# Kernel optimization log

Measured on AMD Instinct MI355X. Metric: run time of the kernel, lower is better.

## Reference

```python
import jax, jax.numpy as jnp
import numpy as np

C = 96          # channels (= output_dim)
NUM_HEADS = 6
DILS = (1, 2, 3)
KS_ATT = 3      # dilate-attention kernel size
KS_COR = 5      # self-correlation kernel size
PAD_COR = 2
LN_EPS = 1e-5


def _unfold(x, k, dil, pad):
    # torch.nn.Unfold(kernel=k, dilation=dil, padding=pad, stride=1)
    # x: [B, C, H, W] -> [B, C, k*k, H, W] (channel-major, kernel row-major)
    B, c, H, W = x.shape
    xp = jnp.pad(x, ((0, 0), (0, 0), (pad, pad), (pad, pad)))
    patches = [xp[:, :, i * dil:i * dil + H, j * dil:j * dil + W]
               for i in range(k) for j in range(k)]
    return jnp.stack(patches, axis=2)


def _layernorm(x, g, b):
    m = jnp.mean(x, axis=-1, keepdims=True)
    v = jnp.mean((x - m) ** 2, axis=-1, keepdims=True)
    return (x - m) * jax.lax.rsqrt(v + LN_EPS) * g + b


def _dilate_attn(q, k, v, dil, head_dim, scale):
    # q,k,v: [B, cb, H, W] with cb = C // num_dilation
    B, cb, H, W = q.shape
    heads = cb // head_dim
    qf = q.reshape(B, heads, head_dim, H * W)                                  # bhdn
    kp = _unfold(k, KS_ATT, dil, dil).reshape(B, heads, head_dim, KS_ATT * KS_ATT, H * W)
    attn = jax.nn.softmax(jnp.einsum('bhdn,bhdkn->bhnk', qf, kp) * scale, axis=-1)
    vp = _unfold(v, KS_ATT, dil, dil).reshape(B, heads, head_dim, KS_ATT * KS_ATT, H * W)
    out = jnp.einsum('bhnk,bhdkn->bnhd', attn, vp)                             # [B,HW,heads,hd]
    return out.reshape(B, H, W, cb)


def _forward(x, g1, b1, Wqkv, bqkv, Wproj, bproj, g2, b2, W1, bm1, W2, bm2):
    B, Cc, H, W = x.shape
    nd = len(DILS)
    head_dim = Cc // NUM_HEADS
    scale = head_dim ** (-0.5)

    xh = jnp.transpose(x, (0, 2, 3, 1))                                        # [B,H,W,C]

    # --- MultiDilatelocalAttention block ---
    y = _layernorm(xh, g1, b1)
    qkv = jnp.einsum('bhwc,oc->bhwo', y, Wqkv) + bqkv                          # 1x1 conv == linear
    qkv = jnp.transpose(qkv, (0, 3, 1, 2)).reshape(B, 3, nd, Cc // nd, H, W)
    outs = []
    for i, d in enumerate(DILS):
        outs.append(_dilate_attn(qkv[:, 0, i], qkv[:, 1, i], qkv[:, 2, i], d, head_dim, scale))
    a = jnp.concatenate(outs, axis=-1)                                         # dilation-major channels
    a = a @ Wproj.T + bproj
    xh = xh + a

    # --- MLP block ---
    z = _layernorm(xh, g2, b2)
    z = jax.nn.gelu(z @ W1.T + bm1, approximate=False) @ W2.T + bm2
    xh = xh + z

    # --- self-correlation ---
    xc = jnp.transpose(xh, (0, 3, 1, 2))                                       # [B,C,H,W]
    xc = jax.nn.relu(xc)
    nrm = jnp.sqrt(jnp.sum(xc * xc, axis=1, keepdims=True))
    xc = xc / jnp.maximum(nrm, 1e-12)                                          # F.normalize dim=1
    pat = _unfold(xc, KS_COR, 1, PAD_COR)                                      # [B,C,25,H,W]
    out = pat.reshape(B, Cc, KS_COR, KS_COR, H, W) * xc[:, :, None, None]
    return jnp.transpose(out, (0, 1, 4, 5, 2, 3))                              # [B,C,H,W,5,5]


def setup_inputs() -> dict:
    key = jax.random.key(0)
    ks = jax.random.split(key, 8)
    B, H, W = 8, 64, 64
    s = 0.02
    return {
        'x': jax.random.normal(ks[0], (B, C, H, W), jnp.float32),
        'g1': jnp.ones((C,), jnp.float32),
        'b1': jnp.zeros((C,), jnp.float32),
        'Wqkv': jax.random.normal(ks[1], (3 * C, C), jnp.float32) * s,
        'bqkv': jnp.zeros((3 * C,), jnp.float32),
        'Wproj': jax.random.normal(ks[2], (C, C), jnp.float32) * s,
        'bproj': jnp.zeros((C,), jnp.float32),
        'g2': jnp.ones((C,), jnp.float32),
        'b2': jnp.zeros((C,), jnp.float32),
        'W1': jax.random.normal(ks[3], (4 * C, C), jnp.float32) * s,
        'bm1': jnp.zeros((4 * C,), jnp.float32),
        'W2': jax.random.normal(ks[4], (C, 4 * C), jnp.float32) * s,
        'bm2': jnp.zeros((C,), jnp.float32),
    }


def reference(x, g1, b1, Wqkv, bqkv, Wproj, bproj, g2, b2, W1, bm1, W2, bm2):
    return _forward(x, g1, b1, Wqkv, bqkv, Wproj, bproj, g2, b2, W1, bm1, W2, bm2)
```

## Files before the change

kernel.cpp:

```cpp
#include <hip/hip_runtime.h>
#include <math.h>

#define NN 4096
#define BN 32768
#define CSTR 66

using short8 = __attribute__((ext_vector_type(8))) short;
using f32x4  = __attribute__((ext_vector_type(4))) float;
typedef unsigned short ushort_t;

__device__ inline unsigned f2bfu(float f) {
    unsigned u = __builtin_bit_cast(unsigned, f);
    u += 0x7FFFu + ((u >> 16) & 1u);
    return u >> 16;
}
__device__ inline ushort_t f2bf(float f) { return (ushort_t)f2bfu(f); }
__device__ inline unsigned pack2(float a, float b) { return f2bfu(a) | (f2bfu(b) << 16); }
__device__ inline float bflo(unsigned u) { return __builtin_bit_cast(float, u << 16); }
__device__ inline float bfhi(unsigned u) { return __builtin_bit_cast(float, u & 0xFFFF0000u); }

__device__ inline float gelu_f(float v) {
    float xx = v * 0.70710678118654752f;
    float a  = fabsf(xx);
    float t  = 1.0f / (1.0f + 0.3275911f * a);
    float p  = t*(0.254829592f + t*(-0.284496736f + t*(1.421413741f + t*(-1.453152027f + t*1.061405429f))));
    float erfv = 1.0f - p * __expf(-xx*xx);
    erfv = copysignf(erfv, xx);
    return 0.5f * v * (1.0f + erfv);
}

__device__ inline void stage_w(const unsigned* __restrict__ wbf, int stage,
                               ushort_t* dst, int wv, int lane) {
    const unsigned* src = wbf + (long)stage * 5120 + lane * 4;
    #pragma unroll
    for (int i = 0; i < 5; ++i) {
        int chunk = wv + 4 * i;
        __builtin_amdgcn_global_load_lds(
            (const __attribute__((address_space(1))) unsigned*)(src + chunk * 256),
            (__attribute__((address_space(3))) unsigned*)(dst + chunk * 512),
            16, 0, 0);
    }
}

__global__ __launch_bounds__(256) void k0_pack(
    const float* __restrict__ Wqkv, const float* __restrict__ Wproj,
    const float* __restrict__ W1, const float* __restrict__ W2,
    unsigned* __restrict__ wbf)
{
    int d = blockIdx.x * 256 + threadIdx.x;
    int s = d / 5120, r = d - s * 5120;
    int o = r / 52, qp = r - o * 52;
    unsigned val = 0u;
    if (o < 96 && qp < 48) {
        int q = qp * 2;
        float2 w2;
        if (s == 0)      w2 = *(const float2*)&Wqkv[(long)o * 96 + q];
        else if (s == 1) w2 = *(const float2*)&Wqkv[(long)(96 + o) * 96 + q];
        else if (s == 2) w2 = *(const float2*)&Wqkv[(long)(192 + o) * 96 + q];
        else if (s == 3) w2 = *(const float2*)&Wproj[(long)o * 96 + q];
        else if (((s - 4) & 1) == 0) { int kb = (s - 4) >> 1; w2 = *(const float2*)&W1[(long)(kb * 96 + o) * 96 + q]; }
        else                         { int kb = (s - 4) >> 1; w2 = *(const float2*)&W2[(long)o * 384 + kb * 96 + q]; }
        val = pack2(w2.x, w2.y);
    }
    wbf[d] = val;
}

__global__ __launch_bounds__(256, 2) void k1_ln_kv(
    const float* __restrict__ x, const float* __restrict__ g1, const float* __restrict__ b1,
    const float* __restrict__ bqkv, const unsigned* __restrict__ wbf,
    unsigned* __restrict__ kvt32)
{
    __shared__ __align__(16) float    Cs[96 * CSTR];
    __shared__ __align__(16) ushort_t As[64 * 104];
    __shared__ __align__(16) ushort_t Bs[2][10240];
    __shared__ float lnm[64], lnr[64];
    const int tid = threadIdx.x;
    const int bid = blockIdx.x;
    const int wg  = ((bid & 7) << 6) | (bid >> 3);
    const long bn0 = (long)wg << 6;
    const int b  = (int)(bn0 >> 12);
    const int n0 = (int)(bn0 & 4095);
    const int lane = tid & 63, wv = tid >> 6;
    const int ln = lane & 15, qd = lane >> 4;

    stage_w(wbf, 1, &Bs[0][0], wv, lane);
    stage_w(wbf, 2, &Bs[1][0], wv, lane);
    for (int i = 0; i < 24; ++i) {
        int idx = i * 256 + tid;
        int c = idx >> 6, p = idx & 63;
        Cs[c * CSTR + p] = x[((long)(b * 96 + c) << 12) + n0 + p];
    }
    __syncthreads();
    {
        int p = tid >> 2, part = tid & 3, c0 = part * 24;
        float s = 0.f, ss = 0.f;
        for (int c = c0; c < c0 + 24; ++c) { float v = Cs[c*CSTR + p]; s += v; ss += v*v; }
        s  += __shfl_xor(s, 1);  s  += __shfl_xor(s, 2);
        ss += __shfl_xor(ss, 1); ss += __shfl_xor(ss, 2);
        float m = s * (1.f/96.f);
        float rstd = rsqrtf(ss * (1.f/96.f) - m*m + 1e-5f);
        if (part == 0) { lnm[p] = m; lnr[p] = rstd; }
    }
    __syncthreads();
    for (int i = 0; i < 12; ++i) {
        int idx = i * 256 + tid;
        int p = idx / 48, cp = idx % 48;
        float m = lnm[p], rs = lnr[p];
        int c = 2 * cp;
        *(unsigned*)&As[p * 104 + 2*cp] =
            pack2((Cs[c*CSTR + p]     - m) * rs * g1[c]   + b1[c],
                  (Cs[(c+1)*CSTR + p] - m) * rs * g1[c+1] + b1[c+1]);
    }
    __syncthreads();
    f32x4 acck[6], accv[6];
    #pragma unroll
    for (int t = 0; t < 6; ++t) { acck[t] = (f32x4){0.f,0.f,0.f,0.f}; accv[t] = (f32x4){0.f,0.f,0.f,0.f}; }
    #pragma unroll
    for (int kc = 0; kc < 3; ++kc) {
        short8 a = *(const short8*)&As[(wv*16 + ln)*104 + kc*32 + qd*8];
        #pragma unroll
        for (int t = 0; t < 6; ++t) {
            short8 bf = *(const short8*)&Bs[0][(t*16 + ln)*104 + kc*32 + qd*8];
            acck[t] = __builtin_amdgcn_mfma_f32_16x16x32_bf16(a, bf, acck[t], 0, 0, 0);
        }
    }
    #pragma unroll
    for (int t = 0; t < 6; ++t)
        #pragma unroll
        for (int r = 0; r < 4; ++r)
            Cs[(t*16 + ln)*CSTR + (wv*16 + qd*4 + r)] = acck[t][r];
    __syncthreads();
    #pragma unroll
    for (int kc = 0; kc < 3; ++kc) {
        short8 a = *(const short8*)&As[(wv*16 + ln)*104 + kc*32 + qd*8];
        #pragma unroll
        for (int t = 0; t < 6; ++t) {
            short8 bf = *(const short8*)&Bs[1][(t*16 + ln)*104 + kc*32 + qd*8];
            accv[t] = __builtin_amdgcn_mfma_f32_16x16x32_bf16(a, bf, accv[t], 0, 0, 0);
        }
    }
    for (int i = 0; i < 12; ++i) {
        int idx = i * 256 + tid;
        int cp = idx / 64, p = idx % 64;
        int c = 2 * cp;
        kvt32[((long)(b*96 + cp) << 12) + n0 + p] =
            pack2(Cs[c*CSTR + p] + bqkv[96 + c], Cs[(c+1)*CSTR + p] + bqkv[96 + c + 1]);
    }
    __syncthreads();
    #pragma unroll
    for (int t = 0; t < 6; ++t)
        #pragma unroll
        for (int r = 0; r < 4; ++r)
            Cs[(t*16 + ln)*CSTR + (wv*16 + qd*4 + r)] = accv[t][r];
    __syncthreads();
    for (int i = 0; i < 12; ++i) {
        int idx = i * 256 + tid;
        int cp = idx / 64, p = idx % 64;
        int c = 2 * cp;
        kvt32[((long)(b*96 + 48 + cp) << 12) + n0 + p] =
            pack2(Cs[c*CSTR + p] + bqkv[192 + c], Cs[(c+1)*CSTR + p] + bqkv[192 + c + 1]);
    }
}

__global__ __launch_bounds__(256, 2) void k2345(
    const unsigned* __restrict__ kvt32, const float* __restrict__ x,
    const float* __restrict__ g1, const float* __restrict__ b1,
    const float* __restrict__ bqkv, const unsigned* __restrict__ wbf,
    const float* __restrict__ bproj,
    const float* __restrict__ g2, const float* __restrict__ b2,
    const float* __restrict__ bm1, const float* __restrict__ bm2,
    float* __restrict__ xcn)
{
    __shared__ __align__(16) float    Cs[96 * CSTR];
    __shared__ __align__(16) ushort_t As[64 * 104];
    __shared__ __align__(16) ushort_t Bs[2][10240];
    __shared__ float lnm[64], lnr[64];
    ushort_t* Hs = (ushort_t*)Cs;
    const int tid = threadIdx.x;
    const int bid = blockIdx.x;
    const int wg  = ((bid & 7) << 6) | (bid >> 3);
    const long bn0 = (long)wg << 6;
    const int b  = (int)(bn0 >> 12);
    const int n0 = (int)(bn0 & 4095);
    const int h0 = n0 >> 6;
    const int lane = tid & 63, wv = tid >> 6;
    const int ln = lane & 15, qd = lane >> 4;

    stage_w(wbf, 0, &Bs[0][0], wv, lane);
    stage_w(wbf, 3, &Bs[1][0], wv, lane);
    for (int i = 0; i < 24; ++i) {
        int idx = i * 256 + tid;
        int c = idx >> 6, p = idx & 63;
        Cs[c * CSTR + p] = x[((long)(b * 96 + c) << 12) + n0 + p];
    }
    __syncthreads();
    {
        int p = tid >> 2, part = tid & 3, c0 = part * 24;
        float s = 0.f, ss = 0.f;
        for (int c = c0; c < c0 + 24; ++c) { float v = Cs[c*CSTR + p]; s += v; ss += v*v; }
        s  += __shfl_xor(s, 1);  s  += __shfl_xor(s, 2);
        ss += __shfl_xor(ss, 1); ss += __shfl_xor(ss, 2);
        float m = s * (1.f/96.f);
        float rstd = rsqrtf(ss * (1.f/96.f) - m*m + 1e-5f);
        if (part == 0) { lnm[p] = m; lnr[p] = rstd; }
    }
    __syncthreads();
    for (int i = 0; i < 12; ++i) {
        int idx = i * 256 + tid;
        int p = idx / 48, cp = idx % 48;
        float m = lnm[p], rs = lnr[p];
        int c = 2 * cp;
        *(unsigned*)&As[p * 104 + 2*cp] =
            pack2((Cs[c*CSTR + p]     - m) * rs * g1[c]   + b1[c],
                  (Cs[(c+1)*CSTR + p] - m) * rs * g1[c+1] + b1[c+1]);
    }
    __syncthreads();
    {
        f32x4 acc[6];
        #pragma unroll
        for (int t = 0; t < 6; ++t) acc[t] = (f32x4){0.f,0.f,0.f,0.f};
        #pragma unroll
        for (int kc = 0; kc < 3; ++kc) {
            short8 a = *(const short8*)&As[(wv*16 + ln)*104 + kc*32 + qd*8];
            #pragma unroll
            for (int t = 0; t < 6; ++t) {
                short8 bf = *(const short8*)&Bs[0][(t*16 + ln)*104 + kc*32 + qd*8];
                acc[t] = __builtin_amdgcn_mfma_f32_16x16x32_bf16(a, bf, acc[t], 0, 0, 0);
            }
        }
        #pragma unroll
        for (int t = 0; t < 6; ++t) {
            float bias = bqkv[t*16 + ln];
            #pragma unroll
            for (int r = 0; r < 4; ++r)
                As[(wv*16 + qd*4 + r)*104 + t*16 + ln] = f2bf(acc[t][r] + bias);
        }
    }
    __syncthreads();
    stage_w(wbf, 4, &Bs[0][0], wv, lane);
    for (int it = 0; it < 2; ++it) {
        int item = it * 256 + tid;
        if (item < 384) {
            int p = item & 63;
            int r = item >> 6;
            int head = r & 1, di = r >> 1;
            int dil = di + 1;
            int cp0 = di*16 + head*8;
            const unsigned* K = kvt32 + ((long)(b*96 +      cp0) << 12);
            const unsigned* V = kvt32 + ((long)(b*96 + 48 + cp0) << 12);
            int w = p;

            float q[16];
            #pragma unroll
            for (int j = 0; j < 8; ++j) {
                unsigned u = *(const unsigned*)&As[p * 104 + 2*(cp0 + j)];
                q[2*j] = bflo(u); q[2*j+1] = bfhi(u);
            }
            float logits[9];
            #pragma unroll
            for (int ki = 0; ki < 3; ++ki)
                #pragma unroll
                for (int kj = 0; kj < 3; ++kj) {
                    int hh = h0 + (ki-1)*dil, ww = w + (kj-1)*dil;
                    float l = 0.f;
                    if ((unsigned)hh < 64u && (unsigned)ww < 64u) {
                        int nn = (hh << 6) + ww;
                        #pragma unroll
                        for (int j = 0; j < 8; ++j) {
                            unsigned u = K[((long)j << 12) + nn];
                            l += q[2*j] * bflo(u) + q[2*j+1] * bfhi(u);
                        }
                    }
                    logits[ki*3 + kj] = l * 0.25f;
                }
            float m = logits[0];
            #pragma unroll
            for (int k = 1; k < 9; ++k) m = fmaxf(m, logits[k]);
            float e[9], s = 0.f;
            #pragma unroll
            for (int k = 0; k < 9; ++k) { e[k] = __expf(logits[k] - m); s += e[k]; }
            float inv = 1.f / s;
            float o[16];
            #pragma unroll
            for (int d = 0; d < 16; ++d) o[d] = 0.f;
            #pragma unroll
            for (int ki = 0; ki < 3; ++ki)
                #pragma unroll
                for (int kj = 0; kj < 3; ++kj) {
                    int hh = h0 + (ki-1)*dil, ww = w + (kj-1)*dil;
                    if ((unsigned)hh < 64u && (unsigned)ww < 64u) {
                        int nn = (hh << 6) + ww;
                        float wgt = e[ki*3 + kj] * inv;
                        #pragma unroll
                        for (int j = 0; j < 8; ++j) {
                            unsigned u = V[((long)j << 12) + nn];
                            o[2*j]   += wgt * bflo(u);
                            o[2*j+1] += wgt * bfhi(u);
                        }
                    }
                }
            #pragma unroll
            for (int j = 0; j < 8; ++j)
                *(unsigned*)&As[p * 104 + 2*(cp0 + j)] = pack2(o[2*j], o[2*j+1]);
        }
    }
    __syncthreads();
    float resid[24];
    {
        f32x4 acc[6];
        #pragma unroll
        for (int t = 0; t < 6; ++t) acc[t] = (f32x4){0.f,0.f,0.f,0.f};
        #pragma unroll
        for (int kc = 0; kc < 3; ++kc) {
            short8 a = *(const short8*)&As[(wv*16 + ln)*104 + kc*32 + qd*8];
            #pragma unroll
            for (int t = 0; t < 6; ++t) {
                short8 bf = *(const short8*)&Bs[1][(t*16 + ln)*104 + kc*32 + qd*8];
                acc[t] = __builtin_amdgcn_mfma_f32_16x16x32_bf16(a, bf, acc[t], 0, 0, 0);
            }
        }
        #pragma unroll
        for (int t = 0; t < 6; ++t) {
            int oc = t*16 + ln;
            float bias = bproj[oc];
            #pragma unroll
            for (int r = 0; r < 4; ++r) {
                int p = wv*16 + qd*4 + r;
                float v = acc[t][r] + bias + Cs[oc*CSTR + p];
                resid[t*4 + r] = v;
                Cs[oc*CSTR + p] = v;
            }
        }
    }
    __syncthreads();
    stage_w(wbf, 5, &Bs[1][0], wv, lane);
    {
        int p = tid >> 2, part = tid & 3, c0 = part * 24;
        float s = 0.f, ss = 0.f;
        for (int c = c0; c < c0 + 24; ++c) { float v = Cs[c*CSTR + p]; s += v; ss += v*v; }
        s  += __shfl_xor(s, 1);  s  += __shfl_xor(s, 2);
        ss += __shfl_xor(ss, 1); ss += __shfl_xor(ss, 2);
        float m = s * (1.f/96.f);
        float rstd = rsqrtf(ss * (1.f/96.f) - m*m + 1e-5f);
        if (part == 0) { lnm[p] = m; lnr[p] = rstd; }
    }
    __syncthreads();
    for (int i = 0; i < 12; ++i) {
        int idx = i * 256 + tid;
        int p = idx / 48, cp = idx % 48;
        float m = lnm[p], rs = lnr[p];
        int c = 2 * cp;
        *(unsigned*)&As[p * 104 + 2*cp] =
            pack2((Cs[c*CSTR + p]     - m) * rs * g2[c]   + b2[c],
                  (Cs[(c+1)*CSTR + p] - m) * rs * g2[c+1] + b2[c+1]);
    }
    __syncthreads();
    f32x4 acc2[6];
    #pragma unroll
    for (int t = 0; t < 6; ++t) acc2[t] = (f32x4){0.f,0.f,0.f,0.f};
    for (int kb = 0; kb < 4; ++kb) {
        f32x4 acch[6];
        #pragma unroll
        for (int t = 0; t < 6; ++t) acch[t] = (f32x4){0.f,0.f,0.f,0.f};
        #pragma unroll
        for (int kc = 0; kc < 3; ++kc) {
            short8 a = *(const short8*)&As[(wv*16 + ln)*104 + kc*32 + qd*8];
            #pragma unroll
            for (int t = 0; t < 6; ++t) {
                short8 bf = *(const short8*)&Bs[0][(t*16 + ln)*104 + kc*32 + qd*8];
                acch[t] = __builtin_amdgcn_mfma_f32_16x16x32_bf16(a, bf, acch[t], 0, 0, 0);
            }
        }
        #pragma unroll
        for (int t = 0; t < 6; ++t) {
            float bias = bm1[kb*96 + t*16 + ln];
            #pragma unroll
            for (int r = 0; r < 4; ++r)
                Hs[(wv*16 + qd*4 + r)*104 + t*16 + ln] = f2bf(gelu_f(acch[t][r] + bias));
        }
        __syncthreads();
        if (kb < 3) stage_w(wbf, 6 + 2*kb, &Bs[0][0], wv, lane);
        #pragma unroll
        for (int kc = 0; kc < 3; ++kc) {
            short8 a = *(const short8*)&Hs[(wv*16 + ln)*104 + kc*32 + qd*8];
            #pragma unroll
            for (int t = 0; t < 6; ++t) {
                short8 bf = *(const short8*)&Bs[1][(t*16 + ln)*104 + kc*32 + qd*8];
                acc2[t] = __builtin_amdgcn_mfma_f32_16x16x32_bf16(a, bf, acc2[t], 0, 0, 0);
            }
        }
        __syncthreads();
        if (kb < 3) stage_w(wbf, 7 + 2*kb, &Bs[1][0], wv, lane);
    }
    #pragma unroll
    for (int t = 0; t < 6; ++t) {
        int oc = t*16 + ln;
        float bias = bm2[oc];
        #pragma unroll
        for (int r = 0; r < 4; ++r) {
            int p = wv*16 + qd*4 + r;
            float v = acc2[t][r] + bias + resid[t*4 + r];
            Cs[oc*CSTR + p] = fmaxf(v, 0.f);
        }
    }
    __syncthreads();
    {
        int p = tid >> 2, part = tid & 3, c0 = part * 24;
        float ss = 0.f;
        for (int c = c0; c < c0 + 24; ++c) { float v = Cs[c*CSTR + p]; ss += v*v; }
        ss += __shfl_xor(ss, 1); ss += __shfl_xor(ss, 2);
        if (part == 0) lnr[p] = 1.f / fmaxf(sqrtf(ss), 1e-12f);
    }
    __syncthreads();
    for (int i = 0; i < 12; ++i) {
        int idx = i * 256 + tid;
        int p = idx / 48, cp = idx % 48;
        float inv = lnr[p];
        float2 v = make_float2(Cs[(2*cp)*CSTR + p] * inv, Cs[(2*cp+1)*CSTR + p] * inv);
        *(float2*)&xcn[(bn0 + p) * 96 + 2*cp] = v;
    }
}

__global__ __launch_bounds__(256) void k6_selfcorr(
    const float* __restrict__ xcn, float* __restrict__ out)
{
    __shared__ float xt[5 * 20 * 97];
    const int tid = threadIdx.x;
    const int wc = blockIdx.x;
    const int h  = blockIdx.y;
    const int b  = blockIdx.z;
    const int w0 = wc * 16;

    for (int i = 0; i < 38; ++i) {
        int idx = i * 256 + tid;
        if (idx < 9600) {
            int r = idx / (20 * 96);
            int rem = idx - r * (20 * 96);
            int wi = rem / 96, c = rem - wi * 96;
            int hh = h + r - 2, ww = w0 + wi - 2;
            float v = 0.f;
            if ((unsigned)hh < 64u && (unsigned)ww < 64u)
                v = xcn[(((long)b << 12) + (hh << 6) + ww) * 96 + c];
            xt[(r * 20 + wi) * 97 + c] = v;
        }
    }
    __syncthreads();
    f32x4* out4 = (f32x4*)out;
    const long ob4 = (long)b * 2457600 + (long)h * 400 + wc * 100;
    for (int i = 0; i < 38; ++i) {
        int idx = i * 256 + tid;
        if (idx < 9600) {
            int c = idx / 100;
            int r4 = idx - c * 100;
            f32x4 v;
            #pragma unroll
            for (int j = 0; j < 4; ++j) {
                int r = r4 * 4 + j;
                int lw = r / 25, k = r - lw * 25;
                int ki = k / 5, kj = k - ki * 5;
                float center = xt[(42 + lw) * 97 + c];
                float neigh  = xt[(ki * 20 + lw + kj) * 97 + c];
                v[j] = center * neigh;
            }
            __builtin_nontemporal_store(v, &out4[ob4 + (long)c * 25600 + r4]);
        }
    }
}

extern "C" void kernel_launch(void* const* d_in, const int* in_sizes, int n_in,
                              void* d_out, int out_size, void* d_ws, size_t ws_size,
                              hipStream_t stream)
{
    const float* x     = (const float*)d_in[0];
    const float* g1    = (const float*)d_in[1];
    const float* b1    = (const float*)d_in[2];
    const float* Wqkv  = (const float*)d_in[3];
    const float* bqkv  = (const float*)d_in[4];
    const float* Wproj = (const float*)d_in[5];
    const float* bproj = (const float*)d_in[6];
    const float* g2    = (const float*)d_in[7];
    const float* b2    = (const float*)d_in[8];
    const float* W1    = (const float*)d_in[9];
    const float* bm1   = (const float*)d_in[10];
    const float* W2    = (const float*)d_in[11];
    const float* bm2   = (const float*)d_in[12];
    float* out = (float*)d_out;

    char* w = (char*)d_ws;
    unsigned* wbf   = (unsigned*)w;  w += 12 * 20480;
    unsigned* kvt32 = (unsigned*)w;  w += (size_t)BN * 192 * 2;
    float*    xcn   = (float*)w;

    k0_pack    <<<240, 256, 0, stream>>>(Wqkv, Wproj, W1, W2, wbf);
    k1_ln_kv   <<<BN / 64, 256, 0, stream>>>(x, g1, b1, bqkv, wbf, kvt32);
    k2345      <<<BN / 64, 256, 0, stream>>>(kvt32, x, g1, b1, bqkv, wbf,
                                             bproj, g2, b2, bm1, bm2, xcn);
    k6_selfcorr<<<dim3(4, 64, 8), 256, 0, stream>>>(xcn, out);
}
```

Baseline: 406.2 us.

## Compute Q in first kernel, store K/V pixel-major for vectorized attention loads

The Q projection moves from the attention kernel into the LN/QKV kernel, which now writes a padded bf16 Q tile image that the second kernel copies straight into LDS. This removes the duplicate LayerNorm and Q GEMM from the second kernel. K/V are now stored pixel-major (96 packed words per pixel) instead of channel-major, so each neighbour's 16-dim head slice is read with two 16-byte loads instead of eight strided 4-byte loads. The x tile load is also vectorized to float4. The cost is an extra global round trip for Q and a less coalesced K/V store in the first kernel.

```diff
diff --git a/kernel.cpp b/kernel.cpp
--- a/kernel.cpp
+++ b/kernel.cpp
@@ -41,6 +41,44 @@
             16, 0, 0);
     }
 }
+
+__device__ inline float dotk16(const unsigned* kv, const float* q) {
+    const uint4 a = *(const uint4*)kv;
+    const uint4 b = *(const uint4*)(kv + 4);
+    float l;
+    l  = q[0]*bflo(a.x)  + q[1]*bfhi(a.x);
+    l += q[2]*bflo(a.y)  + q[3]*bfhi(a.y);
+    l += q[4]*bflo(a.z)  + q[5]*bfhi(a.z);
+    l += q[6]*bflo(a.w)  + q[7]*bfhi(a.w);
+    l += q[8]*bflo(b.x)  + q[9]*bfhi(b.x);
+    l += q[10]*bflo(b.y) + q[11]*bfhi(b.y);
+    l += q[12]*bflo(b.z) + q[13]*bfhi(b.z);
+    l += q[14]*bflo(b.w) + q[15]*bfhi(b.w);
+    return l;
+}
+__device__ inline void accv16(const unsigned* kv, float wgt, float* o) {
+    const uint4 a = *(const uint4*)kv;
+    const uint4 b = *(const uint4*)(kv + 4);
+    o[0]  += wgt*bflo(a.x);  o[1]  += wgt*bfhi(a.x);
+    o[2]  += wgt*bflo(a.y);  o[3]  += wgt*bfhi(a.y);
+    o[4]  += wgt*bflo(a.z);  o[5]  += wgt*bfhi(a.z);
+    o[6]  += wgt*bflo(a.w);  o[7]  += wgt*bfhi(a.w);
+    o[8]  += wgt*bflo(b.x);  o[9]  += wgt*bfhi(b.x);
+    o[10] += wgt*bflo(b.y);  o[11] += wgt*bfhi(b.y);
+    o[12] += wgt*bflo(b.z);  o[13] += wgt*bfhi(b.z);
+    o[14] += wgt*bflo(b.w);  o[15] += wgt*bfhi(b.w);
+}
+
+#define MFMA_GEMM6(ACC, APTR, BPTR)                                              \
+    _Pragma("unroll")                                                            \
+    for (int kc = 0; kc < 3; ++kc) {                                             \
+        short8 a_ = *(const short8*)&(APTR)[(wv*16 + ln)*104 + kc*32 + qd*8];    \
+        _Pragma("unroll")                                                        \
+        for (int t = 0; t < 6; ++t) {                                            \
+            short8 b_ = *(const short8*)&(BPTR)[(t*16 + ln)*104 + kc*32 + qd*8]; \
+            ACC[t] = __builtin_amdgcn_mfma_f32_16x16x32_bf16(a_, b_, ACC[t], 0, 0, 0); \
+        }                                                                        \
+    }
 
 __global__ __launch_bounds__(256) void k0_pack(
     const float* __restrict__ Wqkv, const float* __restrict__ Wproj,
@@ -65,10 +103,10 @@
     wbf[d] = val;
 }
 
-__global__ __launch_bounds__(256, 2) void k1_ln_kv(
+__global__ __launch_bounds__(256, 2) void k1_ln_qkv(
     const float* __restrict__ x, const float* __restrict__ g1, const float* __restrict__ b1,
     const float* __restrict__ bqkv, const unsigned* __restrict__ wbf,
-    unsigned* __restrict__ kvt32)
+    unsigned* __restrict__ kvt32, unsigned* __restrict__ qimg)
 {
     __shared__ __align__(16) float    Cs[96 * CSTR];
     __shared__ __align__(16) ushort_t As[64 * 104];
@@ -83,12 +121,14 @@
     const int lane = tid & 63, wv = tid >> 6;
     const int ln = lane & 15, qd = lane >> 4;
 
-    stage_w(wbf, 1, &Bs[0][0], wv, lane);
-    stage_w(wbf, 2, &Bs[1][0], wv, lane);
-    for (int i = 0; i < 24; ++i) {
-        int idx = i * 256 + tid;
-        int c = idx >> 6, p = idx & 63;
-        Cs[c * CSTR + p] = x[((long)(b * 96 + c) << 12) + n0 + p];
+    stage_w(wbf, 0, &Bs[0][0], wv, lane);
+    stage_w(wbf, 1, &Bs[1][0], wv, lane);
+    for (int i = 0; i < 6; ++i) {
+        int idx = i * 256 + tid;
+        int c = idx >> 4, p4 = idx & 15;
+        float4 v = *(const float4*)&x[((long)(b * 96 + c) << 12) + n0 + p4 * 4];
+        float* dst = &Cs[c * CSTR + p4 * 4];
+        dst[0] = v.x; dst[1] = v.y; dst[2] = v.z; dst[3] = v.w;
     }
     __syncthreads();
     {
@@ -112,60 +152,66 @@
                   (Cs[(c+1)*CSTR + p] - m) * rs * g1[c+1] + b1[c+1]);
     }
     __syncthreads();
-    f32x4 acck[6], accv[6];
-    #pragma unroll
-    for (int t = 0; t < 6; ++t) { acck[t] = (f32x4){0.f,0.f,0.f,0.f}; accv[t] = (f32x4){0.f,0.f,0.f,0.f}; }
-    #pragma unroll
-    for (int kc = 0; kc < 3; ++kc) {
-        short8 a = *(const short8*)&As[(wv*16 + ln)*104 + kc*32 + qd*8];
-        #pragma unroll
-        for (int t = 0; t < 6; ++t) {
-            short8 bf = *(const short8*)&Bs[0][(t*16 + ln)*104 + kc*32 + qd*8];
-            acck[t] = __builtin_amdgcn_mfma_f32_16x16x32_bf16(a, bf, acck[t], 0, 0, 0);
-        }
-    }
+    f32x4 acc[6];
+    #pragma unroll
+    for (int t = 0; t < 6; ++t) acc[t] = (f32x4){0.f,0.f,0.f,0.f};
+    MFMA_GEMM6(acc, As, Bs[0]);
     #pragma unroll
     for (int t = 0; t < 6; ++t)
         #pragma unroll
         for (int r = 0; r < 4; ++r)
-            Cs[(t*16 + ln)*CSTR + (wv*16 + qd*4 + r)] = acck[t][r];
-    __syncthreads();
-    #pragma unroll
-    for (int kc = 0; kc < 3; ++kc) {
-        short8 a = *(const short8*)&As[(wv*16 + ln)*104 + kc*32 + qd*8];
-        #pragma unroll
-        for (int t = 0; t < 6; ++t) {
-            short8 bf = *(const short8*)&Bs[1][(t*16 + ln)*104 + kc*32 + qd*8];
-            accv[t] = __builtin_amdgcn_mfma_f32_16x16x32_bf16(a, bf, accv[t], 0, 0, 0);
-        }
-    }
+            Cs[(t*16 + ln)*CSTR + (wv*16 + qd*4 + r)] = acc[t][r];
+    __syncthreads();
+    stage_w(wbf, 2, &Bs[0][0], wv, lane);
+    for (int i = 0; i < 13; ++i) {
+        int idx = i * 256 + tid;
+        int p = idx / 52, cp = idx - p * 52;
+        unsigned val = 0u;
+        if (cp < 48) {
+            int c = 2 * cp;
+            val = pack2(Cs[c*CSTR + p] + bqkv[c], Cs[(c+1)*CSTR + p] + bqkv[c+1]);
+        }
+        qimg[(long)wg * 3328 + idx] = val;
+    }
+    #pragma unroll
+    for (int t = 0; t < 6; ++t) acc[t] = (f32x4){0.f,0.f,0.f,0.f};
+    MFMA_GEMM6(acc, As, Bs[1]);
+    __syncthreads();
+    #pragma unroll
+    for (int t = 0; t < 6; ++t)
+        #pragma unroll
+        for (int r = 0; r < 4; ++r)
+            Cs[(t*16 + ln)*CSTR + (wv*16 + qd*4 + r)] = acc[t][r];
+    __syncthreads();
     for (int i = 0; i < 12; ++i) {
         int idx = i * 256 + tid;
-        int cp = idx / 64, p = idx % 64;
+        int p = idx / 48, cp = idx % 48;
         int c = 2 * cp;
-        kvt32[((long)(b*96 + cp) << 12) + n0 + p] =
+        kvt32[(bn0 + p) * 96 + cp] =
             pack2(Cs[c*CSTR + p] + bqkv[96 + c], Cs[(c+1)*CSTR + p] + bqkv[96 + c + 1]);
     }
+    #pragma unroll
+    for (int t = 0; t < 6; ++t) acc[t] = (f32x4){0.f,0.f,0.f,0.f};
+    MFMA_GEMM6(acc, As, Bs[0]);
     __syncthreads();
     #pragma unroll
     for (int t = 0; t < 6; ++t)
         #pragma unroll
         for (int r = 0; r < 4; ++r)
-            Cs[(t*16 + ln)*CSTR + (wv*16 + qd*4 + r)] = accv[t][r];
+            Cs[(t*16 + ln)*CSTR + (wv*16 + qd*4 + r)] = acc[t][r];
     __syncthreads();
     for (int i = 0; i < 12; ++i) {
         int idx = i * 256 + tid;
-        int cp = idx / 64, p = idx % 64;
+        int p = idx / 48, cp = idx % 48;
         int c = 2 * cp;
-        kvt32[((long)(b*96 + 48 + cp) << 12) + n0 + p] =
+        kvt32[(bn0 + p) * 96 + 48 + cp] =
             pack2(Cs[c*CSTR + p] + bqkv[192 + c], Cs[(c+1)*CSTR + p] + bqkv[192 + c + 1]);
     }
 }
 
 __global__ __launch_bounds__(256, 2) void k2345(
-    const unsigned* __restrict__ kvt32, const float* __restrict__ x,
-    const float* __restrict__ g1, const float* __restrict__ b1,
-    const float* __restrict__ bqkv, const unsigned* __restrict__ wbf,
+    const unsigned* __restrict__ kvt32, const unsigned* __restrict__ qimg,
+    const float* __restrict__ x, const unsigned* __restrict__ wbf,
     const float* __restrict__ bproj,
     const float* __restrict__ g2, const float* __restrict__ b2,
     const float* __restrict__ bm1, const float* __restrict__ bm2,
@@ -186,14 +232,105 @@
     const int lane = tid & 63, wv = tid >> 6;
     const int ln = lane & 15, qd = lane >> 4;
 
-    stage_w(wbf, 0, &Bs[0][0], wv, lane);
-    stage_w(wbf, 3, &Bs[1][0], wv, lane);
-    for (int i = 0; i < 24; ++i) {
-        int idx = i * 256 + tid;
-        int c = idx >> 6, p = idx & 63;
-        Cs[c * CSTR + p] = x[((long)(b * 96 + c) << 12) + n0 + p];
-    }
-    __syncthreads();
+    stage_w(wbf, 3, &Bs[0][0], wv, lane);
+    stage_w(wbf, 4, &Bs[1][0], wv, lane);
+    {
+        const unsigned* src = qimg + (long)wg * 3328 + lane * 4;
+        #pragma unroll
+        for (int i = 0; i < 4; ++i) {
+            int chunk = wv + 4 * i;
+            if (chunk < 13)
+                __builtin_amdgcn_global_load_lds(
+                    (const __attribute__((address_space(1))) unsigned*)(src + chunk * 256),
+                    (__attribute__((address_space(3))) unsigned*)((ushort_t*)As + chunk * 512),
+                    16, 0, 0);
+        }
+    }
+    for (int i = 0; i < 6; ++i) {
+        int idx = i * 256 + tid;
+        int c = idx >> 4, p4 = idx & 15;
+        float4 v = *(const float4*)&x[((long)(b * 96 + c) << 12) + n0 + p4 * 4];
+        float* dst = &Cs[c * CSTR + p4 * 4];
+        dst[0] = v.x; dst[1] = v.y; dst[2] = v.z; dst[3] = v.w;
+    }
+    __syncthreads();
+    const unsigned* KV = kvt32 + (long)b * 4096 * 96;
+    for (int it = 0; it < 2; ++it) {
+        int item = it * 256 + tid;
+        if (item < 384) {
+            int p = item & 63;
+            int r = item >> 6;
+            int head = r & 1, di = r >> 1;
+            int dil = di + 1;
+            int cp0 = di*16 + head*8;
+            int w = p;
+
+            float q[16];
+            #pragma unroll
+            for (int j = 0; j < 8; ++j) {
+                unsigned u = *(const unsigned*)&As[p * 104 + 2*(cp0 + j)];
+                q[2*j] = bflo(u); q[2*j+1] = bfhi(u);
+            }
+            float logits[9];
+            #pragma unroll
+            for (int ki = 0; ki < 3; ++ki)
+                #pragma unroll
+                for (int kj = 0; kj < 3; ++kj) {
+                    int hh = h0 + (ki-1)*dil, ww = w + (kj-1)*dil;
+                    float l = 0.f;
+                    if ((unsigned)hh < 64u && (unsigned)ww < 64u) {
+                        int nn = (hh << 6) + ww;
+                        l = dotk16(KV + (long)nn * 96 + cp0, q);
+                    }
+                    logits[ki*3 + kj] = l * 0.25f;
+                }
+            float m = logits[0];
+            #pragma unroll
+            for (int k = 1; k < 9; ++k) m = fmaxf(m, logits[k]);
+            float e[9], s = 0.f;
+            #pragma unroll
+            for (int k = 0; k < 9; ++k) { e[k] = __expf(logits[k] - m); s += e[k]; }
+            float inv = 1.f / s;
+            float o[16];
+            #pragma unroll
+            for (int d = 0; d < 16; ++d) o[d] = 0.f;
+            #pragma unroll
+            for (int ki = 0; ki < 3; ++ki)
+                #pragma unroll
+                for (int kj = 0; kj < 3; ++kj) {
+                    int hh = h0 + (ki-1)*dil, ww = w + (kj-1)*dil;
+                    if ((unsigned)hh < 64u && (unsigned)ww < 64u) {
+                        int nn = (hh << 6) + ww;
+                        accv16(KV + (long)nn * 96 + 48 + cp0, e[ki*3 + kj] * inv, o);
+                    }
+                }
+            #pragma unroll
+            for (int j = 0; j < 8; ++j)
+                *(unsigned*)&As[p * 104 + 2*(cp0 + j)] = pack2(o[2*j], o[2*j+1]);
+        }
+    }
+    __syncthreads();
+    float resid[24];
+    {
+        f32x4 acc[6];
+        #pragma unroll
+        for (int t = 0; t < 6; ++t) acc[t] = (f32x4){0.f,0.f,0.f,0.f};
+        MFMA_GEMM6(acc, As, Bs[0]);
+        #pragma unroll
+        for (int t = 0; t < 6; ++t) {
+            int oc = t*16 + ln;
+            float bias = bproj[oc];
+            #pragma unroll
+            for (int r = 0; r < 4; ++r) {
+                int p = wv*16 + qd*4 + r;
+                float v = acc[t][r] + bias + Cs[oc*CSTR + p];
+                resid[t*4 + r] = v;
+                Cs[oc*CSTR + p] = v;
+            }
+        }
+    }
+    __syncthreads();
+    stage_w(wbf, 5, &Bs[0][0], wv, lane);
     {
         int p = tid >> 2, part = tid & 3, c0 = part * 24;
         float s = 0.f, ss = 0.f;
@@ -211,146 +348,6 @@
         float m = lnm[p], rs = lnr[p];
         int c = 2 * cp;
         *(unsigned*)&As[p * 104 + 2*cp] =
-            pack2((Cs[c*CSTR + p]     - m) * rs * g1[c]   + b1[c],
-                  (Cs[(c+1)*CSTR + p] - m) * rs * g1[c+1] + b1[c+1]);
-    }
-    __syncthreads();
-    {
-        f32x4 acc[6];
-        #pragma unroll
-        for (int t = 0; t < 6; ++t) acc[t] = (f32x4){0.f,0.f,0.f,0.f};
-        #pragma unroll
-        for (int kc = 0; kc < 3; ++kc) {
-            short8 a = *(const short8*)&As[(wv*16 + ln)*104 + kc*32 + qd*8];
-            #pragma unroll
-            for (int t = 0; t < 6; ++t) {
-                short8 bf = *(const short8*)&Bs[0][(t*16 + ln)*104 + kc*32 + qd*8];
-                acc[t] = __builtin_amdgcn_mfma_f32_16x16x32_bf16(a, bf, acc[t], 0, 0, 0);
-            }
-        }
-        #pragma unroll
-        for (int t = 0; t < 6; ++t) {
-            float bias = bqkv[t*16 + ln];
-            #pragma unroll
-            for (int r = 0; r < 4; ++r)
-                As[(wv*16 + qd*4 + r)*104 + t*16 + ln] = f2bf(acc[t][r] + bias);
-        }
-    }
-    __syncthreads();
-    stage_w(wbf, 4, &Bs[0][0], wv, lane);
-    for (int it = 0; it < 2; ++it) {
-        int item = it * 256 + tid;
-        if (item < 384) {
-            int p = item & 63;
-            int r = item >> 6;
-            int head = r & 1, di = r >> 1;
-            int dil = di + 1;
-            int cp0 = di*16 + head*8;
-            const unsigned* K = kvt32 + ((long)(b*96 +      cp0) << 12);
-            const unsigned* V = kvt32 + ((long)(b*96 + 48 + cp0) << 12);
-            int w = p;
-
-            float q[16];
-            #pragma unroll
-            for (int j = 0; j < 8; ++j) {
-                unsigned u = *(const unsigned*)&As[p * 104 + 2*(cp0 + j)];
-                q[2*j] = bflo(u); q[2*j+1] = bfhi(u);
-            }
-            float logits[9];
-            #pragma unroll
-            for (int ki = 0; ki < 3; ++ki)
-                #pragma unroll
-                for (int kj = 0; kj < 3; ++kj) {
-                    int hh = h0 + (ki-1)*dil, ww = w + (kj-1)*dil;
-                    float l = 0.f;
-                    if ((unsigned)hh < 64u && (unsigned)ww < 64u) {
-                        int nn = (hh << 6) + ww;
-                        #pragma unroll
-                        for (int j = 0; j < 8; ++j) {
-                            unsigned u = K[((long)j << 12) + nn];
-                            l += q[2*j] * bflo(u) + q[2*j+1] * bfhi(u);
-                        }
-                    }
-                    logits[ki*3 + kj] = l * 0.25f;
-                }
-            float m = logits[0];
-            #pragma unroll
-            for (int k = 1; k < 9; ++k) m = fmaxf(m, logits[k]);
-            float e[9], s = 0.f;
-            #pragma unroll
-            for (int k = 0; k < 9; ++k) { e[k] = __expf(logits[k] - m); s += e[k]; }
-            float inv = 1.f / s;
-            float o[16];
-            #pragma unroll
-            for (int d = 0; d < 16; ++d) o[d] = 0.f;
-            #pragma unroll
-            for (int ki = 0; ki < 3; ++ki)
-                #pragma unroll
-                for (int kj = 0; kj < 3; ++kj) {
-                    int hh = h0 + (ki-1)*dil, ww = w + (kj-1)*dil;
-                    if ((unsigned)hh < 64u && (unsigned)ww < 64u) {
-                        int nn = (hh << 6) + ww;
-                        float wgt = e[ki*3 + kj] * inv;
-                        #pragma unroll
-                        for (int j = 0; j < 8; ++j) {
-                            unsigned u = V[((long)j << 12) + nn];
-                            o[2*j]   += wgt * bflo(u);
-                            o[2*j+1] += wgt * bfhi(u);
-                        }
-                    }
-                }
-            #pragma unroll
-            for (int j = 0; j < 8; ++j)
-                *(unsigned*)&As[p * 104 + 2*(cp0 + j)] = pack2(o[2*j], o[2*j+1]);
-        }
-    }
-    __syncthreads();
-    float resid[24];
-    {
-        f32x4 acc[6];
-        #pragma unroll
-        for (int t = 0; t < 6; ++t) acc[t] = (f32x4){0.f,0.f,0.f,0.f};
-        #pragma unroll
-        for (int kc = 0; kc < 3; ++kc) {
-            short8 a = *(const short8*)&As[(wv*16 + ln)*104 + kc*32 + qd*8];
-            #pragma unroll
-            for (int t = 0; t < 6; ++t) {
-                short8 bf = *(const short8*)&Bs[1][(t*16 + ln)*104 + kc*32 + qd*8];
-                acc[t] = __builtin_amdgcn_mfma_f32_16x16x32_bf16(a, bf, acc[t], 0, 0, 0);
-            }
-        }
-        #pragma unroll
-        for (int t = 0; t < 6; ++t) {
-            int oc = t*16 + ln;
-            float bias = bproj[oc];
-            #pragma unroll
-            for (int r = 0; r < 4; ++r) {
-                int p = wv*16 + qd*4 + r;
-                float v = acc[t][r] + bias + Cs[oc*CSTR + p];
-                resid[t*4 + r] = v;
-                Cs[oc*CSTR + p] = v;
-            }
-        }
-    }
-    __syncthreads();
-    stage_w(wbf, 5, &Bs[1][0], wv, lane);
-    {
-        int p = tid >> 2, part = tid & 3, c0 = part * 24;
-        float s = 0.f, ss = 0.f;
-        for (int c = c0; c < c0 + 24; ++c) { float v = Cs[c*CSTR + p]; s += v; ss += v*v; }
-        s  += __shfl_xor(s, 1);  s  += __shfl_xor(s, 2);
-        ss += __shfl_xor(ss, 1); ss += __shfl_xor(ss, 2);
-        float m = s * (1.f/96.f);
-        float rstd = rsqrtf(ss * (1.f/96.f) - m*m + 1e-5f);
-        if (part == 0) { lnm[p] = m; lnr[p] = rstd; }
-    }
-    __syncthreads();
-    for (int i = 0; i < 12; ++i) {
-        int idx = i * 256 + tid;
-        int p = idx / 48, cp = idx % 48;
-        float m = lnm[p], rs = lnr[p];
-        int c = 2 * cp;
-        *(unsigned*)&As[p * 104 + 2*cp] =
             pack2((Cs[c*CSTR + p]     - m) * rs * g2[c]   + b2[c],
                   (Cs[(c+1)*CSTR + p] - m) * rs * g2[c+1] + b2[c+1]);
     }
@@ -362,15 +359,7 @@
         f32x4 acch[6];
         #pragma unroll
         for (int t = 0; t < 6; ++t) acch[t] = (f32x4){0.f,0.f,0.f,0.f};
-        #pragma unroll
-        for (int kc = 0; kc < 3; ++kc) {
-            short8 a = *(const short8*)&As[(wv*16 + ln)*104 + kc*32 + qd*8];
-            #pragma unroll
-            for (int t = 0; t < 6; ++t) {
-                short8 bf = *(const short8*)&Bs[0][(t*16 + ln)*104 + kc*32 + qd*8];
-                acch[t] = __builtin_amdgcn_mfma_f32_16x16x32_bf16(a, bf, acch[t], 0, 0, 0);
-            }
-        }
+        MFMA_GEMM6(acch, As, Bs[1]);
         #pragma unroll
         for (int t = 0; t < 6; ++t) {
             float bias = bm1[kb*96 + t*16 + ln];
@@ -379,18 +368,10 @@
                 Hs[(wv*16 + qd*4 + r)*104 + t*16 + ln] = f2bf(gelu_f(acch[t][r] + bias));
         }
         __syncthreads();
-        if (kb < 3) stage_w(wbf, 6 + 2*kb, &Bs[0][0], wv, lane);
-        #pragma unroll
-        for (int kc = 0; kc < 3; ++kc) {
-            short8 a = *(const short8*)&Hs[(wv*16 + ln)*104 + kc*32 + qd*8];
-            #pragma unroll
-            for (int t = 0; t < 6; ++t) {
-                short8 bf = *(const short8*)&Bs[1][(t*16 + ln)*104 + kc*32 + qd*8];
-                acc2[t] = __builtin_amdgcn_mfma_f32_16x16x32_bf16(a, bf, acc2[t], 0, 0, 0);
-            }
-        }
+        if (kb < 3) stage_w(wbf, 6 + 2*kb, &Bs[1][0], wv, lane);
+        MFMA_GEMM6(acc2, Hs, Bs[0]);
         __syncthreads();
-        if (kb < 3) stage_w(wbf, 7 + 2*kb, &Bs[1][0], wv, lane);
+        if (kb < 3) stage_w(wbf, 7 + 2*kb, &Bs[0][0], wv, lane);
     }
     #pragma unroll
     for (int t = 0; t < 6; ++t) {
@@ -488,12 +469,13 @@
 
     char* w = (char*)d_ws;
     unsigned* wbf   = (unsigned*)w;  w += 12 * 20480;
-    unsigned* kvt32 = (unsigned*)w;  w += (size_t)BN * 192 * 2;
+    unsigned* kvt32 = (unsigned*)w;  w += (size_t)BN * 96 * 4;
+    unsigned* qimg  = (unsigned*)w;  w += (size_t)512 * 3328 * 4;
     float*    xcn   = (float*)w;
 
     k0_pack    <<<240, 256, 0, stream>>>(Wqkv, Wproj, W1, W2, wbf);
-    k1_ln_kv   <<<BN / 64, 256, 0, stream>>>(x, g1, b1, bqkv, wbf, kvt32);
-    k2345      <<<BN / 64, 256, 0, stream>>>(kvt32, x, g1, b1, bqkv, wbf,
+    k1_ln_qkv  <<<BN / 64, 256, 0, stream>>>(x, g1, b1, bqkv, wbf, kvt32, qimg);
+    k2345      <<<BN / 64, 256, 0, stream>>>(kvt32, qimg, x, wbf,
                                              bproj, g2, b2, bm1, bm2, xcn);
     k6_selfcorr<<<dim3(4, 64, 8), 256, 0, stream>>>(xcn, out);
 }
```

Result: no change. 409.6 us (+0.8%).

## Compute LayerNorm directly into MFMA register fragments and vectorize global loads

Applied to the files above, without the earlier changes.

Each LayerNorm now has every lane compute its row's statistics with cross-lane shuffles and build the bf16 A-operand fragments in registers. This removes the shared-memory As staging, the separate stats pass and several barriers in k1 and k2345. The x tile loads in k1/k2345 and the xcn halo load in k6 switch to float4 global reads. The cost is more register pressure (24 floats per lane plus fragments), which could hurt occupancy under the 2-blocks launch bound.

```diff
diff --git a/kernel.cpp b/kernel.cpp
--- a/kernel.cpp
+++ b/kernel.cpp
@@ -41,6 +41,56 @@
             16, 0, 0);
     }
 }
+
+#define MFMA_GEMM6(ACC, APTR, BPTR)                                              \
+    _Pragma("unroll")                                                            \
+    for (int kc = 0; kc < 3; ++kc) {                                             \
+        short8 a_ = *(const short8*)&(APTR)[(wv*16 + ln)*104 + kc*32 + qd*8];    \
+        _Pragma("unroll")                                                        \
+        for (int t = 0; t < 6; ++t) {                                            \
+            short8 b_ = *(const short8*)&(BPTR)[(t*16 + ln)*104 + kc*32 + qd*8]; \
+            ACC[t] = __builtin_amdgcn_mfma_f32_16x16x32_bf16(a_, b_, ACC[t], 0, 0, 0); \
+        }                                                                        \
+    }
+
+#define MFMA_GEMM6R(ACC, AF, BPTR)                                               \
+    _Pragma("unroll")                                                            \
+    for (int kc = 0; kc < 3; ++kc) {                                             \
+        _Pragma("unroll")                                                        \
+        for (int t = 0; t < 6; ++t) {                                            \
+            short8 b_ = *(const short8*)&(BPTR)[(t*16 + ln)*104 + kc*32 + qd*8]; \
+            ACC[t] = __builtin_amdgcn_mfma_f32_16x16x32_bf16(AF[kc], b_, ACC[t], 0, 0, 0); \
+        }                                                                        \
+    }
+
+#define LN_FRAGS(AF, CS, G, B)                                                   \
+    {                                                                            \
+        const int p_ = wv*16 + ln;                                               \
+        float xv_[24]; float s_ = 0.f, ss_ = 0.f;                                \
+        _Pragma("unroll")                                                        \
+        for (int kc = 0; kc < 3; ++kc)                                           \
+            _Pragma("unroll")                                                    \
+            for (int j = 0; j < 8; ++j) {                                        \
+                float v_ = (CS)[(kc*32 + qd*8 + j)*CSTR + p_];                   \
+                xv_[kc*8+j] = v_; s_ += v_; ss_ += v_*v_;                        \
+            }                                                                    \
+        s_  += __shfl_xor(s_, 16);  s_  += __shfl_xor(s_, 32);                   \
+        ss_ += __shfl_xor(ss_, 16); ss_ += __shfl_xor(ss_, 32);                  \
+        float m_ = s_ * (1.f/96.f);                                              \
+        float rs_ = rsqrtf(ss_ * (1.f/96.f) - m_*m_ + 1e-5f);                    \
+        _Pragma("unroll")                                                        \
+        for (int kc = 0; kc < 3; ++kc)                                           \
+            _Pragma("unroll")                                                    \
+            for (int h = 0; h < 2; ++h) {                                        \
+                int c0_ = kc*32 + qd*8 + h*4;                                    \
+                float4 g4_ = *(const float4*)&(G)[c0_];                          \
+                float4 b4_ = *(const float4*)&(B)[c0_];                          \
+                (AF)[kc][h*4+0] = (short)f2bf((xv_[kc*8+h*4+0]-m_)*rs_*g4_.x + b4_.x); \
+                (AF)[kc][h*4+1] = (short)f2bf((xv_[kc*8+h*4+1]-m_)*rs_*g4_.y + b4_.y); \
+                (AF)[kc][h*4+2] = (short)f2bf((xv_[kc*8+h*4+2]-m_)*rs_*g4_.z + b4_.z); \
+                (AF)[kc][h*4+3] = (short)f2bf((xv_[kc*8+h*4+3]-m_)*rs_*g4_.w + b4_.w); \
+            }                                                                    \
+    }
 
 __global__ __launch_bounds__(256) void k0_pack(
     const float* __restrict__ Wqkv, const float* __restrict__ Wproj,
@@ -71,9 +121,7 @@
     unsigned* __restrict__ kvt32)
 {
     __shared__ __align__(16) float    Cs[96 * CSTR];
-    __shared__ __align__(16) ushort_t As[64 * 104];
     __shared__ __align__(16) ushort_t Bs[2][10240];
-    __shared__ float lnm[64], lnr[64];
     const int tid = threadIdx.x;
     const int bid = blockIdx.x;
     const int wg  = ((bid & 7) << 6) | (bid >> 3);
@@ -85,60 +133,30 @@
 
     stage_w(wbf, 1, &Bs[0][0], wv, lane);
     stage_w(wbf, 2, &Bs[1][0], wv, lane);
-    for (int i = 0; i < 24; ++i) {
-        int idx = i * 256 + tid;
-        int c = idx >> 6, p = idx & 63;
-        Cs[c * CSTR + p] = x[((long)(b * 96 + c) << 12) + n0 + p];
-    }
-    __syncthreads();
-    {
-        int p = tid >> 2, part = tid & 3, c0 = part * 24;
-        float s = 0.f, ss = 0.f;
-        for (int c = c0; c < c0 + 24; ++c) { float v = Cs[c*CSTR + p]; s += v; ss += v*v; }
-        s  += __shfl_xor(s, 1);  s  += __shfl_xor(s, 2);
-        ss += __shfl_xor(ss, 1); ss += __shfl_xor(ss, 2);
-        float m = s * (1.f/96.f);
-        float rstd = rsqrtf(ss * (1.f/96.f) - m*m + 1e-5f);
-        if (part == 0) { lnm[p] = m; lnr[p] = rstd; }
-    }
-    __syncthreads();
-    for (int i = 0; i < 12; ++i) {
-        int idx = i * 256 + tid;
-        int p = idx / 48, cp = idx % 48;
-        float m = lnm[p], rs = lnr[p];
-        int c = 2 * cp;
-        *(unsigned*)&As[p * 104 + 2*cp] =
-            pack2((Cs[c*CSTR + p]     - m) * rs * g1[c]   + b1[c],
-                  (Cs[(c+1)*CSTR + p] - m) * rs * g1[c+1] + b1[c+1]);
-    }
-    __syncthreads();
-    f32x4 acck[6], accv[6];
-    #pragma unroll
-    for (int t = 0; t < 6; ++t) { acck[t] = (f32x4){0.f,0.f,0.f,0.f}; accv[t] = (f32x4){0.f,0.f,0.f,0.f}; }
-    #pragma unroll
-    for (int kc = 0; kc < 3; ++kc) {
-        short8 a = *(const short8*)&As[(wv*16 + ln)*104 + kc*32 + qd*8];
-        #pragma unroll
-        for (int t = 0; t < 6; ++t) {
-            short8 bf = *(const short8*)&Bs[0][(t*16 + ln)*104 + kc*32 + qd*8];
-            acck[t] = __builtin_amdgcn_mfma_f32_16x16x32_bf16(a, bf, acck[t], 0, 0, 0);
-        }
-    }
+    for (int i = 0; i < 6; ++i) {
+        int idx = i * 256 + tid;
+        int c = idx >> 4, p4 = idx & 15;
+        float4 v = *(const float4*)&x[((long)(b * 96 + c) << 12) + n0 + p4 * 4];
+        float* dst = &Cs[c * CSTR + p4 * 4];
+        dst[0] = v.x; dst[1] = v.y; dst[2] = v.z; dst[3] = v.w;
+    }
+    __syncthreads();
+    short8 af[3];
+    LN_FRAGS(af, Cs, g1, b1);
+    f32x4 acck[6];
+    #pragma unroll
+    for (int t = 0; t < 6; ++t) acck[t] = (f32x4){0.f,0.f,0.f,0.f};
+    MFMA_GEMM6R(acck, af, Bs[0]);
+    __syncthreads();
     #pragma unroll
     for (int t = 0; t < 6; ++t)
         #pragma unroll
         for (int r = 0; r < 4; ++r)
             Cs[(t*16 + ln)*CSTR + (wv*16 + qd*4 + r)] = acck[t][r];
     __syncthreads();
-    #pragma unroll
-    for (int kc = 0; kc < 3; ++kc) {
-        short8 a = *(const short8*)&As[(wv*16 + ln)*104 + kc*32 + qd*8];
-        #pragma unroll
-        for (int t = 0; t < 6; ++t) {
-            short8 bf = *(const short8*)&Bs[1][(t*16 + ln)*104 + kc*32 + qd*8];
-            accv[t] = __builtin_amdgcn_mfma_f32_16x16x32_bf16(a, bf, accv[t], 0, 0, 0);
-        }
-    }
+    f32x4 accv[6];
+    #pragma unroll
+    for (int t = 0; t < 6; ++t) accv[t] = (f32x4){0.f,0.f,0.f,0.f};
     for (int i = 0; i < 12; ++i) {
         int idx = i * 256 + tid;
         int cp = idx / 64, p = idx % 64;
@@ -146,6 +164,7 @@
         kvt32[((long)(b*96 + cp) << 12) + n0 + p] =
             pack2(Cs[c*CSTR + p] + bqkv[96 + c], Cs[(c+1)*CSTR + p] + bqkv[96 + c + 1]);
     }
+    MFMA_GEMM6R(accv, af, Bs[1]);
     __syncthreads();
     #pragma unroll
     for (int t = 0; t < 6; ++t)
@@ -174,7 +193,7 @@
     __shared__ __align__(16) float    Cs[96 * CSTR];
     __shared__ __align__(16) ushort_t As[64 * 104];
     __shared__ __align__(16) ushort_t Bs[2][10240];
-    __shared__ float lnm[64], lnr[64];
+    __shared__ float lnr[64];
     ushort_t* Hs = (ushort_t*)Cs;
     const int tid = threadIdx.x;
     const int bid = blockIdx.x;
@@ -188,46 +207,21 @@
 
     stage_w(wbf, 0, &Bs[0][0], wv, lane);
     stage_w(wbf, 3, &Bs[1][0], wv, lane);
-    for (int i = 0; i < 24; ++i) {
-        int idx = i * 256 + tid;
-        int c = idx >> 6, p = idx & 63;
-        Cs[c * CSTR + p] = x[((long)(b * 96 + c) << 12) + n0 + p];
+    for (int i = 0; i < 6; ++i) {
+        int idx = i * 256 + tid;
+        int c = idx >> 4, p4 = idx & 15;
+        float4 v = *(const float4*)&x[((long)(b * 96 + c) << 12) + n0 + p4 * 4];
+        float* dst = &Cs[c * CSTR + p4 * 4];
+        dst[0] = v.x; dst[1] = v.y; dst[2] = v.z; dst[3] = v.w;
     }
     __syncthreads();
     {
-        int p = tid >> 2, part = tid & 3, c0 = part * 24;
-        float s = 0.f, ss = 0.f;
-        for (int c = c0; c < c0 + 24; ++c) { float v = Cs[c*CSTR + p]; s += v; ss += v*v; }
-        s  += __shfl_xor(s, 1);  s  += __shfl_xor(s, 2);
-        ss += __shfl_xor(ss, 1); ss += __shfl_xor(ss, 2);
-        float m = s * (1.f/96.f);
-        float rstd = rsqrtf(ss * (1.f/96.f) - m*m + 1e-5f);
-        if (part == 0) { lnm[p] = m; lnr[p] = rstd; }
-    }
-    __syncthreads();
-    for (int i = 0; i < 12; ++i) {
-        int idx = i * 256 + tid;
-        int p = idx / 48, cp = idx % 48;
-        float m = lnm[p], rs = lnr[p];
-        int c = 2 * cp;
-        *(unsigned*)&As[p * 104 + 2*cp] =
-            pack2((Cs[c*CSTR + p]     - m) * rs * g1[c]   + b1[c],
-                  (Cs[(c+1)*CSTR + p] - m) * rs * g1[c+1] + b1[c+1]);
-    }
-    __syncthreads();
-    {
+        short8 af[3];
+        LN_FRAGS(af, Cs, g1, b1);
         f32x4 acc[6];
         #pragma unroll
         for (int t = 0; t < 6; ++t) acc[t] = (f32x4){0.f,0.f,0.f,0.f};
-        #pragma unroll
-        for (int kc = 0; kc < 3; ++kc) {
-            short8 a = *(const short8*)&As[(wv*16 + ln)*104 + kc*32 + qd*8];
-            #pragma unroll
-            for (int t = 0; t < 6; ++t) {
-                short8 bf = *(const short8*)&Bs[0][(t*16 + ln)*104 + kc*32 + qd*8];
-                acc[t] = __builtin_amdgcn_mfma_f32_16x16x32_bf16(a, bf, acc[t], 0, 0, 0);
-            }
-        }
+        MFMA_GEMM6R(acc, af, Bs[0]);
         #pragma unroll
         for (int t = 0; t < 6; ++t) {
             float bias = bqkv[t*16 + ln];
@@ -310,15 +304,7 @@
         f32x4 acc[6];
         #pragma unroll
         for (int t = 0; t < 6; ++t) acc[t] = (f32x4){0.f,0.f,0.f,0.f};
-        #pragma unroll
-        for (int kc = 0; kc < 3; ++kc) {
-            short8 a = *(const short8*)&As[(wv*16 + ln)*104 + kc*32 + qd*8];
-            #pragma unroll
-            for (int t = 0; t < 6; ++t) {
-                short8 bf = *(const short8*)&Bs[1][(t*16 + ln)*104 + kc*32 + qd*8];
-                acc[t] = __builtin_amdgcn_mfma_f32_16x16x32_bf16(a, bf, acc[t], 0, 0, 0);
-            }
-        }
+        MFMA_GEMM6(acc, As, Bs[1]);
         #pragma unroll
         for (int t = 0; t < 6; ++t) {
             int oc = t*16 + ln;
@@ -334,26 +320,8 @@
     }
     __syncthreads();
     stage_w(wbf, 5, &Bs[1][0], wv, lane);
-    {
-        int p = tid >> 2, part = tid & 3, c0 = part * 24;
-        float s = 0.f, ss = 0.f;
-        for (int c = c0; c < c0 + 24; ++c) { float v = Cs[c*CSTR + p]; s += v; ss += v*v; }
-        s  += __shfl_xor(s, 1);  s  += __shfl_xor(s, 2);
-        ss += __shfl_xor(ss, 1); ss += __shfl_xor(ss, 2);
-        float m = s * (1.f/96.f);
-        float rstd = rsqrtf(ss * (1.f/96.f) - m*m + 1e-5f);
-        if (part == 0) { lnm[p] = m; lnr[p] = rstd; }
-    }
-    __syncthreads();
-    for (int i = 0; i < 12; ++i) {
-        int idx = i * 256 + tid;
-        int p = idx / 48, cp = idx % 48;
-        float m = lnm[p], rs = lnr[p];
-        int c = 2 * cp;
-        *(unsigned*)&As[p * 104 + 2*cp] =
-            pack2((Cs[c*CSTR + p]     - m) * rs * g2[c]   + b2[c],
-                  (Cs[(c+1)*CSTR + p] - m) * rs * g2[c+1] + b2[c+1]);
-    }
+    short8 zf[3];
+    LN_FRAGS(zf, Cs, g2, b2);
     __syncthreads();
     f32x4 acc2[6];
     #pragma unroll
@@ -362,15 +330,7 @@
         f32x4 acch[6];
         #pragma unroll
         for (int t = 0; t < 6; ++t) acch[t] = (f32x4){0.f,0.f,0.f,0.f};
-        #pragma unroll
-        for (int kc = 0; kc < 3; ++kc) {
-            short8 a = *(const short8*)&As[(wv*16 + ln)*104 + kc*32 + qd*8];
-            #pragma unroll
-            for (int t = 0; t < 6; ++t) {
-                short8 bf = *(const short8*)&Bs[0][(t*16 + ln)*104 + kc*32 + qd*8];
-                acch[t] = __builtin_amdgcn_mfma_f32_16x16x32_bf16(a, bf, acch[t], 0, 0, 0);
-            }
-        }
+        MFMA_GEMM6R(acch, zf, Bs[0]);
         #pragma unroll
         for (int t = 0; t < 6; ++t) {
             float bias = bm1[kb*96 + t*16 + ln];
@@ -380,15 +340,7 @@
         }
         __syncthreads();
         if (kb < 3) stage_w(wbf, 6 + 2*kb, &Bs[0][0], wv, lane);
-        #pragma unroll
-        for (int kc = 0; kc < 3; ++kc) {
-            short8 a = *(const short8*)&Hs[(wv*16 + ln)*104 + kc*32 + qd*8];
-            #pragma unroll
-            for (int t = 0; t < 6; ++t) {
-                short8 bf = *(const short8*)&Bs[1][(t*16 + ln)*104 + kc*32 + qd*8];
-                acc2[t] = __builtin_amdgcn_mfma_f32_16x16x32_bf16(a, bf, acc2[t], 0, 0, 0);
-            }
-        }
+        MFMA_GEMM6(acc2, Hs, Bs[1]);
         __syncthreads();
         if (kb < 3) stage_w(wbf, 7 + 2*kb, &Bs[1][0], wv, lane);
     }
@@ -431,17 +383,19 @@
     const int b  = blockIdx.z;
     const int w0 = wc * 16;
 
-    for (int i = 0; i < 38; ++i) {
-        int idx = i * 256 + tid;
-        if (idx < 9600) {
-            int r = idx / (20 * 96);
-            int rem = idx - r * (20 * 96);
-            int wi = rem / 96, c = rem - wi * 96;
+    const f32x4* xcn4 = (const f32x4*)xcn;
+    for (int i = 0; i < 10; ++i) {
+        int idx = i * 256 + tid;
+        if (idx < 2400) {
+            int r = idx / 480;
+            int rem = idx - r * 480;
+            int wi = rem / 24, c4 = rem - wi * 24;
             int hh = h + r - 2, ww = w0 + wi - 2;
-            float v = 0.f;
+            f32x4 v = (f32x4){0.f, 0.f, 0.f, 0.f};
             if ((unsigned)hh < 64u && (unsigned)ww < 64u)
-                v = xcn[(((long)b << 12) + (hh << 6) + ww) * 96 + c];
-            xt[(r * 20 + wi) * 97 + c] = v;
+                v = xcn4[(((long)b << 12) + (hh << 6) + ww) * 24 + c4];
+            float* dst = &xt[(r * 20 + wi) * 97 + c4 * 4];
+            dst[0] = v[0]; dst[1] = v[1]; dst[2] = v[2]; dst[3] = v[3];
         }
     }
     __syncthreads();
```

Result: faster. 396.0 us (-2.5%).
